# Kernel tuning notes

Measured on AMD Instinct MI355X. Metric: run time of the kernel, lower is better.

Reference implementation:

```python
import jax, jax.numpy as jnp
import numpy as np

B = 131072
FLOW_SIZE = 16
PASS = 8
TRANS = FLOW_SIZE - PASS  # 8
N_BINS = 128
HIDDEN = 256


def setup_inputs() -> dict:
    key = jax.random.key(0)
    k0, k1, k2 = jax.random.split(key, 3)
    x = jax.random.uniform(k0, (B, FLOW_SIZE + 1), dtype=jnp.float32)
    W1 = jax.random.normal(k1, (PASS, HIDDEN), dtype=jnp.float32) * 0.3
    b1 = jnp.zeros((HIDDEN,), dtype=jnp.float32)
    W2 = jax.random.normal(k2, (HIDDEN, TRANS * N_BINS), dtype=jnp.float32) * 0.05
    b2 = jnp.zeros((TRANS * N_BINS,), dtype=jnp.float32)
    return {"x": x, "W1": W1, "b1": b1, "W2": W2, "b2": b2}


def reference(x, W1, b1, W2, b2):
    xA = x[:, :PASS]                      # [B, P]
    xB = x[:, PASS:FLOW_SIZE]             # [B, T]
    jacobian = x[:, FLOW_SIZE:FLOW_SIZE + 1]  # [B, 1]

    # NN: small MLP, exp output -> positive unnormalized bin widths Q [B, T, n_bins]
    h = jax.nn.relu(xA @ W1 + b1)
    Q = jnp.exp(h @ W2 + b2).reshape(x.shape[0], TRANS, N_BINS)

    Qsum = jnp.cumsum(Q, axis=-1)                     # [B, T, n_bins]
    Qnorms = Qsum[:, :, -1:]                          # [B, T, 1]
    Q = Q / (Qnorms / N_BINS)                         # normalized slopes
    Qsum = Qsum / Qnorms                              # normalized CDF
    Qsum = jnp.pad(Qsum, ((0, 0), (0, 0), (1, 0)))    # left-pad CDF with 0

    alphas = xB * N_BINS
    bins = jnp.floor(alphas)
    alphas = (alphas - bins) / N_BINS                 # fractional offset within bin
    bins = jnp.clip(bins.astype(jnp.int32), 0, N_BINS - 1)

    cdf_int_part = jnp.take_along_axis(Qsum, bins[..., None], axis=-1)[..., 0]  # [B, T]
    cdf_float_part = jnp.take_along_axis(Q, bins[..., None], axis=-1)[..., 0]   # [B, T]

    cdf = cdf_float_part * alphas + cdf_int_part      # [B, T]
    jacobian = jacobian * jnp.prod(cdf_float_part, axis=-1, keepdims=True)  # [B, 1]

    return jnp.concatenate((xA, cdf, jacobian), axis=-1)  # [B, flow_size+1]
```

## Files before the change

kernel.cpp:

```cpp
#include <hip/hip_runtime.h>
#include <math.h>

#define NROWS 131072
#define XC    17
#define ROWSB 64
#define HID   256
#define NB    128
#define NCOL  1024
#define LOG2E 1.44269504088896340736f

typedef __attribute__((ext_vector_type(8))) short bf16x8;
typedef __attribute__((ext_vector_type(4))) float f32x4;

#if __has_builtin(__builtin_amdgcn_exp2f)
#define EXP2F(v) __builtin_amdgcn_exp2f(v)
#else
#define EXP2F(v) exp2f(v)
#endif
#if __has_builtin(__builtin_amdgcn_rcpf)
#define RCPF(v) __builtin_amdgcn_rcpf(v)
#else
#define RCPF(v) (1.f / (v))
#endif

__device__ __forceinline__ unsigned short f2bf(float f) {
    unsigned int u = __float_as_uint(f);
    return (unsigned short)((u + 0x7FFFu + ((u >> 16) & 1u)) >> 16);
}

__device__ __forceinline__ float red16(float v) {
    int x;
    x = __builtin_amdgcn_update_dpp(0, __float_as_int(v), 0xB1, 0xF, 0xF, true);
    v += __int_as_float(x);
    x = __builtin_amdgcn_update_dpp(0, __float_as_int(v), 0x4E, 0xF, 0xF, true);
    v += __int_as_float(x);
    x = __builtin_amdgcn_update_dpp(0, __float_as_int(v), 0x141, 0xF, 0xF, true);
    v += __int_as_float(x);
    x = __builtin_amdgcn_update_dpp(0, __float_as_int(v), 0x140, 0xF, 0xF, true);
    v += __int_as_float(x);
    return v;
}

__global__ void prep_w2(const float* __restrict__ W2, unsigned short* __restrict__ w2t) {
    __shared__ __align__(16) unsigned short tkT[32][80];
    const int tid = threadIdx.x;
    const int k0 = (blockIdx.x & 3) * 64;
    const int c0 = (blockIdx.x >> 2) * 32;
    const int c4 = (tid & 7) * 4;
    const int kk = (tid >> 3) * 2;
    const float4 r0 = *(const float4*)&W2[(size_t)(k0 + kk) * NCOL + c0 + c4];
    const float4 r1 = *(const float4*)&W2[(size_t)(k0 + kk + 1) * NCOL + c0 + c4];
    const float v0[4] = {r0.x, r0.y, r0.z, r0.w};
    const float v1[4] = {r1.x, r1.y, r1.z, r1.w};
    #pragma unroll
    for (int i = 0; i < 4; ++i) {
        const unsigned int p = (unsigned int)f2bf(v0[i] * LOG2E)
                             | ((unsigned int)f2bf(v1[i] * LOG2E) << 16);
        *(unsigned int*)&tkT[c4 + i][kk] = p;
    }
    __syncthreads();
    const int g = tid & 7, c = tid >> 3;
    const uint4 q = *(const uint4*)&tkT[c][g * 8];
    *(uint4*)&w2t[(size_t)(c0 + c) * HID + k0 + ((g ^ (c & 7)) << 3)] = q;
}

__global__ __launch_bounds__(256, 4)
void gplc6(const float* __restrict__ x,
           const float* __restrict__ W1,
           const float* __restrict__ b1,
           const unsigned short* __restrict__ w2t,
           const float* __restrict__ b2,
           float* __restrict__ out)
{
    __shared__ float xs[ROWSB * XC];
    __shared__ __align__(16) union {
        unsigned short hb[32 * HID];
        struct {
            unsigned short w2[4][64 * 64];
            unsigned short b2s[NCOL];
        } g;
    } u;

    const int tid  = threadIdx.x;
    const int lane = tid & 63;
    const int w    = tid >> 6;
    const int quad = lane >> 4;
    const int l15  = lane & 15;
    const int wr   = w * 16;
    const int ksw  = (lane & 7) << 3;
    const size_t r0 = (size_t)blockIdx.x * ROWSB;

    for (int i = tid; i < ROWSB * XC; i += 256) xs[i] = x[r0 * XC + i];
    const int cp = tid & 127, hlf = tid >> 7;
    float w1r[16];
    #pragma unroll
    for (int i = 0; i < 8; ++i) {
        const float2 t2 = *(const float2*)&W1[i * HID + 2 * cp];
        w1r[2 * i] = t2.x; w1r[2 * i + 1] = t2.y;
    }
    const float2 b1v = *(const float2*)&b1[2 * cp];
    __syncthreads();

    bf16x8 afr[8];
    #pragma unroll
    for (int ch = 0; ch < 2; ++ch) {
        for (int r = 0; r < 16; ++r) {
            const int lrow = hlf * 16 + r;
            const int row  = ch * 32 + lrow;
            float a0 = b1v.x, a1 = b1v.y;
            #pragma unroll
            for (int i = 0; i < 8; ++i) {
                const float xv = xs[row * XC + i];
                a0 = fmaf(xv, w1r[2 * i], a0);
                a1 = fmaf(xv, w1r[2 * i + 1], a1);
            }
            a0 = fmaxf(a0, 0.f); a1 = fmaxf(a1, 0.f);
            const int eidx = lrow * HID + (((cp >> 2) ^ (row & 15)) << 3) + ((cp & 3) << 1);
            *(unsigned int*)&u.hb[eidx] = (unsigned int)f2bf(a0) | ((unsigned int)f2bf(a1) << 16);
        }
        __syncthreads();
        if ((w >> 1) == ch) {
            #pragma unroll
            for (int kf = 0; kf < 8; ++kf) {
                const int row = wr + l15;
                afr[kf] = *(const bf16x8*)&u.hb[(row & 31) * HID + (((kf * 4 + quad) ^ l15) << 3)];
            }
        }
        __syncthreads();
    }

    for (int i = tid; i < NCOL; i += 256) u.g.b2s[i] = f2bf(b2[i] * LOG2E);
    asm volatile("s_waitcnt lgkmcnt(0)" ::: "memory");
    __builtin_amdgcn_sched_barrier(0);

    auto stage = [&](int m) {
        const int t = m >> 3, cj = (m >> 2) & 1, buf = m & 3;
        #pragma unroll
        for (int j = 0; j < 2; ++j) {
            const int ci  = (w * 2 + j) * 8 + (lane >> 3);
            const int col = t * NB + cj * 64 + ci;
            const int kl  = (lane & 7) << 3;
            const unsigned short* gp = w2t + (size_t)col * HID + buf * 64 + kl;
            unsigned short* lp = &u.g.w2[buf][(w * 2 + j) * 512];
            __builtin_amdgcn_global_load_lds(
                (const __attribute__((address_space(1))) unsigned int*)gp,
                (__attribute__((address_space(3))) unsigned int*)lp, 16, 0, 0);
        }
    };

    float jf[4] = {1.f, 1.f, 1.f, 1.f};

    stage(0); stage(1); stage(2);
    #pragma unroll 1
    for (int t = 0; t < 8; ++t) {
        f32x4 acc[8];
        #pragma unroll
        for (int ct = 0; ct < 8; ++ct) acc[ct] = (f32x4){0.f, 0.f, 0.f, 0.f};

        #pragma unroll
        for (int cj = 0; cj < 2; ++cj) {
            #pragma unroll
            for (int kc = 0; kc < 4; ++kc) {
                const int m = t * 8 + cj * 4 + kc;
                if (cj == 1 && kc == 2) {
                    if (t == 7) { asm volatile("s_waitcnt vmcnt(2)" ::: "memory"); }
                    else        { asm volatile("s_waitcnt vmcnt(4)" ::: "memory"); }
                } else if (cj == 1 && kc == 3) {
                    if (t == 7) { asm volatile("s_waitcnt vmcnt(0)" ::: "memory"); }
                    else        { asm volatile("s_waitcnt vmcnt(4)" ::: "memory"); }
                } else {
                    asm volatile("s_waitcnt vmcnt(4)" ::: "memory");
                }
                __builtin_amdgcn_s_barrier();
                if (m <= 60) stage(m + 3);

                __builtin_amdgcn_s_setprio(1);
                const unsigned short* wsb = u.g.w2[kc];
                #pragma unroll
                for (int ks = 0; ks < 2; ++ks) {
                    const int kf = kc * 2 + ks;
                    const int klog = ks * 32 + quad * 8;
                    #pragma unroll
                    for (int ci = 0; ci < 4; ++ci) {
                        const int ct = cj * 4 + ci;
                        const int c  = ci * 16 + l15;
                        const bf16x8 bf = *(const bf16x8*)&wsb[c * 64 + (klog ^ ksw)];
                        acc[ct] = __builtin_amdgcn_mfma_f32_16x16x32_bf16(afr[kf], bf, acc[ct], 0, 0, 0);
                    }
                }
                __builtin_amdgcn_s_setprio(0);
            }
        }

        float bb[8];
        #pragma unroll
        for (int ct = 0; ct < 8; ++ct)
            bb[ct] = __uint_as_float((unsigned int)u.g.b2s[t * NB + ct * 16 + l15] << 16);
        #pragma unroll
        for (int i = 0; i < 4; ++i) {
            const int row = wr + quad * 4 + i;
            const float alpha = xs[row * XC + 8 + t] * 128.f;
            const float fb = floorf(alpha);
            const int bin = min(max((int)fb, 0), 127);
            const float fr = alpha - fb;
            float e[8];
            #pragma unroll
            for (int ct = 0; ct < 8; ++ct) e[ct] = EXP2F(acc[ct][i] + bb[ct]);
            const float P1 = e[0],      P2 = P1 + e[1], P3 = P2 + e[2], P4 = P3 + e[3];
            const float P5 = P4 + e[4], P6 = P5 + e[5], P7 = P6 + e[6], P8 = P7 + e[7];
            int thr = (bin - l15 + 15) >> 4;
            thr = min(max(thr, 0), 8);
            const float sA = (thr & 1) ? P1 : 0.f;
            const float sB = (thr & 1) ? P3 : P2;
            const float sC = (thr & 1) ? P5 : P4;
            const float sD = (thr & 1) ? P7 : P6;
            const float sE = (thr & 2) ? sB : sA;
            const float sF = (thr & 2) ? sD : sC;
            float num = (thr & 4) ? sF : sE;
            num = (thr >= 8) ? P8 : num;
            const int cb = bin >> 4;
            const float t1 = (cb & 1) ? e[1] : e[0];
            const float t2 = (cb & 1) ? e[3] : e[2];
            const float t3 = (cb & 1) ? e[5] : e[4];
            const float t4 = (cb & 1) ? e[7] : e[6];
            const float u1 = (cb & 2) ? t2 : t1;
            const float u2 = (cb & 2) ? t4 : t3;
            const float es = (cb & 4) ? u2 : u1;
            float eb  = ((bin & 15) == l15) ? es : 0.f;
            float tot = P8;
            tot = red16(tot); num = red16(num); eb = red16(eb);
            const float inv = RCPF(tot);
            jf[i] *= 128.f * eb * inv;
            if (l15 == 0) xs[row * XC + 8 + t] = fmaf(eb, fr, num) * inv;
        }
    }

    if (l15 == 0) {
        #pragma unroll
        for (int i = 0; i < 4; ++i) {
            const int row = wr + quad * 4 + i;
            xs[row * XC + 16] *= jf[i];
        }
    }
    __syncthreads();
    for (int i = tid; i < ROWSB * XC; i += 256) out[r0 * XC + i] = xs[i];
}

extern "C" void kernel_launch(void* const* d_in, const int* in_sizes, int n_in,
                              void* d_out, int out_size, void* d_ws, size_t ws_size,
                              hipStream_t stream) {
    (void)in_sizes; (void)n_in; (void)ws_size; (void)out_size;
    prep_w2<<<128, 256, 0, stream>>>((const float*)d_in[3], (unsigned short*)d_ws);
    gplc6<<<NROWS / ROWSB, 256, 0, stream>>>(
        (const float*)d_in[0], (const float*)d_in[1], (const float*)d_in[2],
        (const unsigned short*)d_ws, (const float*)d_in[4], (float*)d_out);
}
```

Baseline: 168.4 us.

## Double-buffer W2 LDS fragments in registers and tighten the barrier schedule

Restructures the MFMA inner loop so the B-operand fragments for the next k-chunk are read from LDS into a second register set while the current chunk's MFMAs run. Load-wait and barrier points move after each subphase, and the wait thresholds change from vmcnt(4) to vmcnt(2). The aim is to hide LDS read latency behind matrix-core work. The extra 16 bf16x8 registers push register pressure up, so launch bounds drop from 4 to 3 waves per SIMD, which costs occupancy.

Result: slower. 183.2 us (+8.8%).

```diff
diff --git a/kernel.cpp b/kernel.cpp
--- a/kernel.cpp
+++ b/kernel.cpp
@@ -64,7 +64,7 @@
     *(uint4*)&w2t[(size_t)(c0 + c) * HID + k0 + ((g ^ (c & 7)) << 3)] = q;
 }
 
-__global__ __launch_bounds__(256, 4)
+__global__ __launch_bounds__(256, 3)
 void gplc6(const float* __restrict__ x,
            const float* __restrict__ W1,
            const float* __restrict__ b1,
@@ -148,49 +148,67 @@
         }
     };
 
+    auto prefetch = [&](bf16x8* dst, int bi) {
+        const unsigned short* wsb = u.g.w2[bi];
+        #pragma unroll
+        for (int ks = 0; ks < 2; ++ks) {
+            const int klog = ks * 32 + quad * 8;
+            #pragma unroll
+            for (int ci = 0; ci < 4; ++ci) {
+                const int c = ci * 16 + l15;
+                dst[ks * 4 + ci] = *(const bf16x8*)&wsb[c * 64 + (klog ^ ksw)];
+            }
+        }
+    };
+
     float jf[4] = {1.f, 1.f, 1.f, 1.f};
+    bf16x8 pA[8], pB[8];
+    f32x4 acc[8];
+
+#define SUBPHASE(N, CUR, NXT)                                                   \
+    {                                                                           \
+        const int m_ = t * 8 + (N);                                             \
+        if (m_ <= 60) stage(m_ + 3);                                            \
+        if (m_ < 63) prefetch(NXT, ((N) + 1) & 3);                              \
+        __builtin_amdgcn_s_setprio(1);                                          \
+        _Pragma("unroll")                                                       \
+        for (int ks = 0; ks < 2; ++ks) {                                        \
+            _Pragma("unroll")                                                   \
+            for (int ci = 0; ci < 4; ++ci) {                                    \
+                acc[(((N) >> 2) & 1) * 4 + ci] =                                \
+                    __builtin_amdgcn_mfma_f32_16x16x32_bf16(                    \
+                        afr[((N) & 3) * 2 + ks], CUR[ks * 4 + ci],              \
+                        acc[(((N) >> 2) & 1) * 4 + ci], 0, 0, 0);               \
+            }                                                                   \
+        }                                                                       \
+        __builtin_amdgcn_s_setprio(0);                                          \
+    }
+
+#define WB(N)                                                                   \
+    {                                                                           \
+        if (t < 7 || (N) <= 4) { asm volatile("s_waitcnt vmcnt(2)" ::: "memory"); } \
+        else                   { asm volatile("s_waitcnt vmcnt(0)" ::: "memory"); } \
+        __builtin_amdgcn_s_barrier();                                           \
+    }
 
     stage(0); stage(1); stage(2);
+    asm volatile("s_waitcnt vmcnt(2)" ::: "memory");
+    __builtin_amdgcn_s_barrier();
+    prefetch(pA, 0);
+
     #pragma unroll 1
     for (int t = 0; t < 8; ++t) {
-        f32x4 acc[8];
         #pragma unroll
         for (int ct = 0; ct < 8; ++ct) acc[ct] = (f32x4){0.f, 0.f, 0.f, 0.f};
 
-        #pragma unroll
-        for (int cj = 0; cj < 2; ++cj) {
-            #pragma unroll
-            for (int kc = 0; kc < 4; ++kc) {
-                const int m = t * 8 + cj * 4 + kc;
-                if (cj == 1 && kc == 2) {
-                    if (t == 7) { asm volatile("s_waitcnt vmcnt(2)" ::: "memory"); }
-                    else        { asm volatile("s_waitcnt vmcnt(4)" ::: "memory"); }
-                } else if (cj == 1 && kc == 3) {
-                    if (t == 7) { asm volatile("s_waitcnt vmcnt(0)" ::: "memory"); }
-                    else        { asm volatile("s_waitcnt vmcnt(4)" ::: "memory"); }
-                } else {
-                    asm volatile("s_waitcnt vmcnt(4)" ::: "memory");
-                }
-                __builtin_amdgcn_s_barrier();
-                if (m <= 60) stage(m + 3);
-
-                __builtin_amdgcn_s_setprio(1);
-                const unsigned short* wsb = u.g.w2[kc];
-                #pragma unroll
-                for (int ks = 0; ks < 2; ++ks) {
-                    const int kf = kc * 2 + ks;
-                    const int klog = ks * 32 + quad * 8;
-                    #pragma unroll
-                    for (int ci = 0; ci < 4; ++ci) {
-                        const int ct = cj * 4 + ci;
-                        const int c  = ci * 16 + l15;
-                        const bf16x8 bf = *(const bf16x8*)&wsb[c * 64 + (klog ^ ksw)];
-                        acc[ct] = __builtin_amdgcn_mfma_f32_16x16x32_bf16(afr[kf], bf, acc[ct], 0, 0, 0);
-                    }
-                }
-                __builtin_amdgcn_s_setprio(0);
-            }
-        }
+        SUBPHASE(0, pA, pB) WB(0)
+        SUBPHASE(1, pB, pA) WB(1)
+        SUBPHASE(2, pA, pB) WB(2)
+        SUBPHASE(3, pB, pA) WB(3)
+        SUBPHASE(4, pA, pB) WB(4)
+        SUBPHASE(5, pB, pA) WB(5)
+        SUBPHASE(6, pA, pB) WB(6)
+        SUBPHASE(7, pB, pA)
 
         float bb[8];
         #pragma unroll
@@ -233,7 +251,10 @@
             jf[i] *= 128.f * eb * inv;
             if (l15 == 0) xs[row * XC + 8 + t] = fmaf(eb, fr, num) * inv;
         }
-    }
+        if (t < 7) WB(7)
+    }
+#undef SUBPHASE
+#undef WB
 
     if (l15 == 0) {
         #pragma unroll
```
